# Performance work log

Hardware: AMD Instinct MI355X
Metric: run time of the kernel (lower is better)

## Reference

```python
import jax, jax.numpy as jnp
import numpy as np

B, N, D, H = 8, 512, 1024, 16
HD = D // H
NI = 4          # num_instances == num_instances_per_batch
MAXI = 16       # max_instances
SCALE = HD ** -0.5


def _rms(t, w, eps=1e-6):
    return t * jax.lax.rsqrt(jnp.mean(t * t, axis=-1, keepdims=True) + eps) * w


def _lin(t, W, b):
    return t @ W + b


def _heads(t):
    b, n = t.shape[0], t.shape[1]
    return t.reshape(b, n, H, HD).transpose(0, 2, 1, 3)  # [b, H, n, hd]


def setup_inputs() -> dict:
    key = jax.random.key(0)
    ks = iter(jax.random.split(key, 16))

    def w(shape):
        return jax.random.normal(next(ks), shape, dtype=jnp.float32) * 0.02

    return {
        "x": jax.random.normal(next(ks), (B, N, D), dtype=jnp.float32),
        "instance_mask": jax.random.uniform(next(ks), (B, N, NI), dtype=jnp.float32),
        "Wq": w((D, D)), "bq": jnp.zeros((D,), jnp.float32),
        "Wk": w((D, D)), "bk": jnp.zeros((D,), jnp.float32),
        "Wv": w((D, D)), "bv": jnp.zeros((D,), jnp.float32),
        "Wo": w((D, D)), "bo": jnp.zeros((D,), jnp.float32),
        "Wiq": w((D, D)), "biq": jnp.zeros((D,), jnp.float32),
        "Wik": w((D, D)), "bik": jnp.zeros((D,), jnp.float32),
        "instance_embed": w((1, MAXI, D)),
        "qnorm_w": jnp.ones((HD,), jnp.float32),
        "knorm_w": jnp.ones((HD,), jnp.float32),
        "num_instances": NI,
        "num_instances_per_batch": NI,
    }


def reference(x, instance_mask, Wq, bq, Wk, bk, Wv, bv, Wo, bo,
              Wiq, biq, Wik, bik, instance_embed, qnorm_w, knorm_w,
              num_instances, num_instances_per_batch):
    # QKV projections + per-head QK-RMSNorm
    q = _rms(_heads(_lin(x, Wq, bq)), qnorm_w)   # [B,H,N,hd]
    k = _rms(_heads(_lin(x, Wk, bk)), knorm_w)
    v = _heads(_lin(x, Wv, bv))
    ni = num_instances                           # == num_instances_per_batch here,
    G = B // num_instances_per_batch             # so no leftover self-attn sub-branch;
    # (the module's initial global attention output is overwritten by this branch)
    qg = q.reshape(G, ni, H, N, HD)
    kg = k.reshape(G, ni, H, N, HD).transpose(0, 2, 1, 3, 4).reshape(G, H, ni * N, HD)
    vg = v.reshape(G, ni, H, N, HD).transpose(0, 2, 1, 3, 4).reshape(G, H, ni * N, HD)
    scores = jnp.einsum('gihnd,ghmd->gihnm', qg, kg) * SCALE  # [G,ni,H,N,ni*N]
    p = jax.nn.softmax(scores, axis=-1)
    og = jnp.einsum('gihnm,ghmd->gihnd', p, vg)
    out = og.reshape(B, H, N, HD).transpose(0, 2, 1, 3).reshape(B, N, D)
    # instance-embedding gate
    inst_feat = jnp.einsum('bnk,kd->bnd', instance_mask, instance_embed[0, :ni])
    iq = _heads(_lin(out, Wiq, biq))
    ik = _heads(_lin(inst_feat, Wik, bik))
    # mean over heads folded into the einsum (same math as mean of per-head scores)
    inst_attn = jax.nn.sigmoid(jnp.einsum('bhnd,bhmd->bnm', iq, ik) * (SCALE / H))
    gate = 1.0 + jnp.mean(inst_attn, axis=-1, keepdims=True)  # [B,N,1]
    return _lin(out * gate, Wo, bo)
```

## Files before the change

kernel.cpp:

```cpp
#include <hip/hip_runtime.h>
#include <cmath>

#define B_   8
#define N_   512
#define D_   1024
#define H_   16
#define HD_  64
#define NI_  4
#define BN_  (B_*N_)
#define KVLEN (NI_*N_)

typedef __attribute__((ext_vector_type(8)))  short  bf16x8;
typedef __attribute__((ext_vector_type(8)))  __bf16 bf16x8_t;
typedef __attribute__((ext_vector_type(16))) float  f32x16;
typedef __attribute__((ext_vector_type(4)))  short  s16x4;
typedef __attribute__((ext_vector_type(2)))  unsigned u32x2;

__device__ __forceinline__ short bf16_rn(float x) {
  unsigned u = __float_as_uint(x);
  unsigned r = (u + 0x7FFFu + ((u >> 16) & 1u)) >> 16;
  return (short)r;
}

__device__ __forceinline__ void split2(float x, short& hi, short& lo) {
  hi = bf16_rn(x);
  float h = __uint_as_float(((unsigned)(unsigned short)hi) << 16);
  float r = x - h;
  lo = bf16_rn(r);
}

__device__ __forceinline__ f32x16 mfma_bf16(bf16x8 a, bf16x8 b, f32x16 c) {
  return __builtin_amdgcn_mfma_f32_32x32x16_bf16(
      __builtin_bit_cast(bf16x8_t, a), __builtin_bit_cast(bf16x8_t, b), c, 0, 0, 0);
}

#define GLOAD16(gp, lp) __builtin_amdgcn_global_load_lds( \
  (const __attribute__((address_space(1))) unsigned*)(gp), \
  (__attribute__((address_space(3))) unsigned*)(lp), 16, 0, 0)

__device__ __forceinline__ long tiled_off(int row, int k) {
  return ((((long)(row >> 7) * 128 + (k >> 3)) * 128 + (row & 127)) * 8 + (k & 7));
}

__device__ __forceinline__ void xcd_swizzle(int& bx, int& by, int& bz) {
  const int gx = gridDim.x, gy = gridDim.y;
  const int nwg = gx * gy * gridDim.z;
  const int lin = blockIdx.x + gx * (blockIdx.y + gy * blockIdx.z);
  const int swz = (lin & 7) * (nwg >> 3) + (lin >> 3);
  bx = swz % gx;
  const int rest = swz / gx;
  by = rest % gy;
  bz = rest / gy;
}

__global__ __launch_bounds__(256) void wsplitAll(
    const float* __restrict__ Wq, const float* __restrict__ Wk,
    const float* __restrict__ Wv, const float* __restrict__ Wiq,
    const float* __restrict__ Wik, const float* __restrict__ Wo,
    short* __restrict__ QKVh, short* __restrict__ Gateh)
{
  __shared__ float tile[64][65];
  const int z = blockIdx.z;
  const float* W = (z == 0) ? Wq : (z == 1) ? Wk : (z == 2) ? Wv
                 : (z == 3) ? Wiq : (z == 4) ? Wik : Wo;
  const int t  = threadIdx.x;
  const int kb = blockIdx.y * 64;
  const int cb = blockIdx.x * 64;
  const int r0 = t >> 4;
  const int c4 = t & 15;
  #pragma unroll
  for (int i = 0; i < 4; i++) {
    const int r = r0 + i * 16;
    *(float4*)&tile[r][c4 * 4] = *(const float4*)&W[(long)(kb + r) * D_ + cb + c4 * 4];
  }
  __syncthreads();
  #pragma unroll
  for (int i = 0; i < 4; i++) {
    const int c = r0 + i * 16;
    short hi[4];
    #pragma unroll
    for (int e = 0; e < 4; e++)
      hi[e] = bf16_rn(tile[c4 * 4 + e][c]);
    if (z < 3) {
      *(s16x4*)&QKVh[tiled_off(z * D_ + cb + c, kb + c4 * 4)] = *(s16x4*)hi;
    } else {
      *(s16x4*)&Gateh[(long)(z - 3) * D_ * D_ + tiled_off(cb + c, kb + c4 * 4)] = *(s16x4*)hi;
    }
  }
}

__global__ __launch_bounds__(256) void asplit(const float* __restrict__ in,
                                              short* __restrict__ hi)
{
  const long i4 = ((long)blockIdx.x * 256 + threadIdx.x) * 4;
  const int row = (int)(i4 >> 10);
  const int kk  = (int)(i4 & 1023);
  float4 v = *(const float4*)&in[i4];
  short h[4];
  h[0] = bf16_rn(v.x);
  h[1] = bf16_rn(v.y);
  h[2] = bf16_rn(v.z);
  h[3] = bf16_rn(v.w);
  *(s16x4*)&hi[tiled_off(row, kk)] = *(s16x4*)h;
}

template<int MODE, int SPLIT>
__global__ __launch_bounds__(256) void mfgemm2(
    const short* __restrict__ Ahi, const short* __restrict__ Alo,
    const short* __restrict__ Bhi, const short* __restrict__ Blo,
    const float* __restrict__ b0, const float* __restrict__ b1,
    const float* __restrict__ b2,
    float* __restrict__ C, short* __restrict__ Chi, short* __restrict__ Clo,
    int aBlk, int bBlk, long sC,
    const float* __restrict__ gate_in)
{
  constexpr int NOPS = (SPLIT == 2) ? 3 : 2;
  __shared__ short lds[2][NOPS][4096];
  const int t = threadIdx.x, w = t >> 6, lane = t & 63;
  int bx, by, bz;
  xcd_swizzle(bx, by, bz);
  const int rowBase = by * 128;
  const int colBase = bx * 128;
  const int batch = (MODE == 5) ? (bz >> 1) : bz;
  const long kOff = (MODE == 5) ? (long)(bz & 1) * 65536 : 0;
  const long aoff = (long)(batch * aBlk + by) * 131072 + kOff;
  const long boff = (long)(batch * bBlk + bx) * 131072 + kOff;

  const short* Abase = (MODE == 4 && bz) ? Alo : Ahi;
  const short* Bbase = (MODE == 4 && bz) ? Blo : Bhi;

  const short* mySrc;
  int op, half;
  if (SPLIT == 2) {
    op = (w < 3) ? w : 0; half = 0;
    mySrc = (w == 0) ? Ahi + aoff : (w == 1) ? Alo + aoff : Bhi + boff;
  } else {
    op = w >> 1; half = w & 1;
    mySrc = op ? Bbase + boff : Abase + aoff;
  }

  auto stage = [&](int buf, int tt) {
    if (SPLIT == 2) {
      if (w == 3) return;
      const short* g = mySrc + ((long)tt * 512 + lane) * 8;
      #pragma unroll
      for (int i = 0; i < 8; i++)
        GLOAD16(g + i * 512, &lds[buf][op][i * 512]);
    } else {
      const short* g = mySrc + ((long)tt * 512 + half * 256 + lane) * 8;
      #pragma unroll
      for (int i = 0; i < 4; i++)
        GLOAD16(g + i * 512, &lds[buf][op][(half * 256 + i * 64) * 8]);
    }
  };

  const int wr = w >> 1, wc = w & 1;
  const int lrow = lane & 31, lk = lane >> 5;

  f32x16 acc[2][2] = {};

  auto compute = [&](int buf) {
    #pragma unroll
    for (int kh = 0; kh < 2; kh++) {
      const int kq = 2 * kh + lk;
      bf16x8 ah[2], bh[2];
      #pragma unroll
      for (int m = 0; m < 2; m++)
        ah[m] = *(const bf16x8*)&lds[buf][0][(kq * 128 + wr * 64 + m * 32 + lrow) * 8];
      #pragma unroll
      for (int n = 0; n < 2; n++)
        bh[n] = *(const bf16x8*)&lds[buf][(SPLIT == 2) ? 2 : 1][(kq * 128 + wc * 64 + n * 32 + lrow) * 8];
      if (SPLIT == 2) {
        bf16x8 al[2];
        #pragma unroll
        for (int m = 0; m < 2; m++)
          al[m] = *(const bf16x8*)&lds[buf][1][(kq * 128 + wr * 64 + m * 32 + lrow) * 8];
        #pragma unroll
        for (int m = 0; m < 2; m++)
          #pragma unroll
          for (int n = 0; n < 2; n++) {
            acc[m][n] = mfma_bf16(al[m], bh[n], acc[m][n]);
            acc[m][n] = mfma_bf16(ah[m], bh[n], acc[m][n]);
          }
      } else {
        #pragma unroll
        for (int m = 0; m < 2; m++)
          #pragma unroll
          for (int n = 0; n < 2; n++)
            acc[m][n] = mfma_bf16(ah[m], bh[n], acc[m][n]);
      }
    }
  };

  const int NT = (MODE == 5) ? 16 : 32;
  stage(0, 0);
  for (int tt = 0; tt < NT - 1; ++tt) {
    stage((tt + 1) & 1, tt + 1);
    if (SPLIT == 2) asm volatile("s_waitcnt vmcnt(8)" ::: "memory");
    else            asm volatile("s_waitcnt vmcnt(4)" ::: "memory");
    __builtin_amdgcn_s_barrier();
    __builtin_amdgcn_sched_barrier(0);
    compute(tt & 1);
    __builtin_amdgcn_s_barrier();
  }
  asm volatile("s_waitcnt vmcnt(0)" ::: "memory");
  __builtin_amdgcn_s_barrier();
  __builtin_amdgcn_sched_barrier(0);
  compute((NT - 1) & 1);

  if (MODE == 5) {
    float* Cz = C + (long)(bz & 1) * (8L * 512 * 512) + (long)batch * (512L * 512);
    #pragma unroll
    for (int m = 0; m < 2; m++)
      #pragma unroll
      for (int r = 0; r < 16; r++) {
        const int row = rowBase + wr * 64 + m * 32 + (r & 3) + 8 * (r >> 2) + 4 * lk;
        #pragma unroll
        for (int n = 0; n < 2; n++)
          Cz[(long)row * 512 + colBase + wc * 64 + n * 32 + lrow] = acc[m][n][r];
      }
    return;
  }

  const float* bias = (bz == 1) ? b1 : (bz == 2) ? b2 : b0;
  float bcol[2];
  #pragma unroll
  for (int n = 0; n < 2; n++)
    bcol[n] = bias[colBase + wc * 64 + n * 32 + lrow];

  float* Cb = C + (long)bz * sC;
  short* Cdst = (MODE == 4 && bz) ? Clo : Chi;

  #pragma unroll
  for (int m = 0; m < 2; m++) {
    #pragma unroll
    for (int r = 0; r < 16; r++) {
      const int row = rowBase + wr * 64 + m * 32 + (r & 3) + 8 * (r >> 2) + 4 * lk;
      float g = 1.f;
      if (MODE == 2) g = gate_in[row];
      #pragma unroll
      for (int n = 0; n < 2; n++) {
        const int col = colBase + wc * 64 + n * 32 + lrow;
        const float val = acc[m][n][r] * g + bcol[n];
        if (MODE == 4) {
          Cdst[tiled_off(row, col)] = bf16_rn(val);
        } else {
          Cb[(long)row * D_ + col] = val;
        }
      }
    }
  }
}

__global__ __launch_bounds__(256) void gate_finish(
    const float* __restrict__ zp, float* __restrict__ gate)
{
  const int t = threadIdx.x, w = t >> 6, lane = t & 63;
  const int row = blockIdx.x * 4 + w;
  const float* z0 = zp + (long)row * 512;
  const float* z1 = zp + 8L * 512 * 512 + (long)row * 512;
  const float sc = 0.125f / 16.f;
  float4 a0 = *(const float4*)&z0[lane * 8];
  float4 a1 = *(const float4*)&z0[lane * 8 + 4];
  float4 b0 = *(const float4*)&z1[lane * 8];
  float4 b1 = *(const float4*)&z1[lane * 8 + 4];
  float s = 1.f / (1.f + __expf(-(a0.x + b0.x) * sc))
          + 1.f / (1.f + __expf(-(a0.y + b0.y) * sc))
          + 1.f / (1.f + __expf(-(a0.z + b0.z) * sc))
          + 1.f / (1.f + __expf(-(a0.w + b0.w) * sc))
          + 1.f / (1.f + __expf(-(a1.x + b1.x) * sc))
          + 1.f / (1.f + __expf(-(a1.y + b1.y) * sc))
          + 1.f / (1.f + __expf(-(a1.z + b1.z) * sc))
          + 1.f / (1.f + __expf(-(a1.w + b1.w) * sc));
  #pragma unroll
  for (int m = 1; m < 64; m <<= 1) s += __shfl_xor(s, m);
  if (lane == 0) gate[row] = 1.f + s * (1.f / 512.f);
}

__global__ __launch_bounds__(256) void kvprep(
    const float* __restrict__ kf, const float* __restrict__ vf,
    const float* __restrict__ knw, short* __restrict__ Knb,
    short* __restrict__ Vtb)
{
  const int tile = blockIdx.x, h = blockIdx.y, g = blockIdx.z;
  const int t = threadIdx.x;
  const int skv = t >> 3, sg = t & 7;
  const int m  = tile * 32 + skv;
  const int bb = g * NI_ + (m >> 9), nn = m & (N_ - 1);
  const float* kp = kf + ((long)(bb * N_ + nn)) * D_ + h * HD_ + sg * 8;
  float k8[8];
  *(float4*)&k8[0] = *(const float4*)&kp[0];
  *(float4*)&k8[4] = *(const float4*)&kp[4];
  float ks2 = 0.f;
  #pragma unroll
  for (int j = 0; j < 8; j++) ks2 += k8[j] * k8[j];
  ks2 += __shfl_xor(ks2, 1);
  ks2 += __shfl_xor(ks2, 2);
  ks2 += __shfl_xor(ks2, 4);
  const float kr = rsqrtf(ks2 * (1.f / 64.f) + 1e-6f);
  bf16x8 kb;
  #pragma unroll
  for (int j = 0; j < 8; j++) kb[j] = bf16_rn(k8[j] * kr * knw[sg * 8 + j]);
  *(bf16x8*)&Knb[((long)(g * H_ + h) * KVLEN + m) * 64 + ((sg ^ (m & 7)) * 8)] = kb;
  const int vkv = t & 31, vg = t >> 5;
  const int m2  = tile * 32 + vkv;
  const int bb2 = g * NI_ + (m2 >> 9), nn2 = m2 & (N_ - 1);
  const float* vp = vf + ((long)(bb2 * N_ + nn2)) * D_ + h * HD_ + vg * 8;
  float v8[8];
  *(float4*)&v8[0] = *(const float4*)&vp[0];
  *(float4*)&v8[4] = *(const float4*)&vp[4];
  const long vbase = ((long)(g * H_ + h) * 64 + tile) * 2048;
  #pragma unroll
  for (int e = 0; e < 8; e++) {
    const int d = vg * 8 + e;
    Vtb[vbase + d * 32 + (((vkv >> 3) ^ ((d >> 1) & 3)) * 8) + (vkv & 7)] = bf16_rn(v8[e]);
  }
}

__global__ __launch_bounds__(256) void attn3(
    const float* __restrict__ q, const short* __restrict__ Knb,
    const short* __restrict__ Vtb, const float* __restrict__ qnw,
    float* __restrict__ opart, float* __restrict__ lpart)
{
  int qb, h, bz;
  xcd_swizzle(qb, h, bz);
  const int b  = bz >> 1, s = bz & 1;
  const int g  = b >> 2;
  const int t  = threadIdx.x;
  const int w  = t >> 6;
  const int lane = t & 63;
  const int l31 = lane & 31, hi = lane >> 5;

  __shared__ short Kt[2][2048];
  __shared__ short Vt[2][2048];

  const int qrow = qb * 128 + w * 32 + l31;
  const float* qp = q + ((long)b * N_ + qrow) * D_ + h * HD_ + hi * 8;
  float qv[4][8];
  float ss = 0.f;
  #pragma unroll
  for (int c = 0; c < 4; c++) {
    *(float4*)&qv[c][0] = *(const float4*)&qp[c * 16];
    *(float4*)&qv[c][4] = *(const float4*)&qp[c * 16 + 4];
    #pragma unroll
    for (int j = 0; j < 8; j++) ss += qv[c][j] * qv[c][j];
  }
  ss += __shfl_xor(ss, 32);
  const float qr = rsqrtf(ss * (1.f / 64.f) + 1e-6f);
  bf16x8 qf[4];
  #pragma unroll
  for (int c = 0; c < 4; c++)
    #pragma unroll
    for (int j = 0; j < 8; j++)
      qf[c][j] = bf16_rn(qv[c][j] * qr * qnw[c * 16 + hi * 8 + j]);

  const short* Kg = Knb + (long)(g * H_ + h) * KVLEN * 64 + (long)s * 32 * 2048;
  const short* Vg = Vtb + (long)(g * H_ + h) * 64 * 2048 + (long)s * 32 * 2048;

  auto stage = [&](int buf, int i) {
    GLOAD16(Kg + (long)i * 2048 + t * 8, &Kt[buf][w * 512]);
    GLOAD16(Vg + (long)i * 2048 + t * 8, &Vt[buf][w * 512]);
  };

  f32x16 oacc[2] = {};
  float l = 0.f;

  stage(0, 0);
  for (int i = 0; i < 32; ++i) {
    const int buf = i & 1;
    if (i + 1 < 32) {
      stage(buf ^ 1, i + 1);
      asm volatile("s_waitcnt vmcnt(2)" ::: "memory");
    } else {
      asm volatile("s_waitcnt vmcnt(0)" ::: "memory");
    }
    __builtin_amdgcn_s_barrier();
    __builtin_amdgcn_sched_barrier(0);

    f32x16 sc = {};
    #pragma unroll
    for (int c = 0; c < 4; c++) {
      bf16x8 kfr = *(const bf16x8*)&Kt[buf][l31 * 64 + (((2 * c + hi) * 8) ^ ((l31 & 7) << 3))];
      sc = mfma_bf16(kfr, qf[c], sc);
    }
    float p[16];
    #pragma unroll
    for (int r = 0; r < 16; r++) {
      p[r] = exp2f(fmaf(sc[r], 0.1803368801111244f, -11.541560327111961f));
      l += p[r];
    }
    unsigned wd[8];
    #pragma unroll
    for (int i2 = 0; i2 < 8; i2++)
      asm("v_cvt_pk_bf16_f32 %0, %1, %2" : "=v"(wd[i2]) : "v"(p[2 * i2]), "v"(p[2 * i2 + 1]));
    u32x2 r0 = __builtin_amdgcn_permlane32_swap(wd[0], wd[2], false, false);
    u32x2 r1 = __builtin_amdgcn_permlane32_swap(wd[1], wd[3], false, false);
    u32x2 r2 = __builtin_amdgcn_permlane32_swap(wd[4], wd[6], false, false);
    u32x2 r3 = __builtin_amdgcn_permlane32_swap(wd[5], wd[7], false, false);
    int4 f0 = { (int)r0.x, (int)r1.x, (int)r0.y, (int)r1.y };
    int4 f1 = { (int)r2.x, (int)r3.x, (int)r2.y, (int)r3.y };
    #pragma unroll
    for (int n = 0; n < 2; n++) {
      const int d = n * 32 + l31;
      const int fd = (d >> 1) & 3;
      bf16x8 v0 = *(const bf16x8*)&Vt[buf][d * 32 + ((hi ^ fd) * 8)];
      bf16x8 v1 = *(const bf16x8*)&Vt[buf][d * 32 + (((2 | hi) ^ fd) * 8)];
      oacc[n] = mfma_bf16(__builtin_bit_cast(bf16x8, f0), v0, oacc[n]);
      oacc[n] = mfma_bf16(__builtin_bit_cast(bf16x8, f1), v1, oacc[n]);
    }
    __builtin_amdgcn_s_barrier();
  }

  l += __shfl_xor(l, 32);
  #pragma unroll
  for (int r = 0; r < 16; r++) {
    const int qg = qb * 128 + w * 32 + (r & 3) + 8 * (r >> 2) + 4 * hi;
    float* op = opart + ((long)s * BN_ + b * N_ + qg) * D_ + h * HD_ + l31;
    op[0]  = oacc[0][r];
    op[32] = oacc[1][r];
  }
  if (hi == 0)
    lpart[((long)s * BN_ + b * N_ + qb * 128 + w * 32 + l31) * H_ + h] = l;
}

__global__ __launch_bounds__(256) void reduce_if(
    const float* __restrict__ opart, const float* __restrict__ lpart,
    const float* __restrict__ mask, const float* __restrict__ emb,
    short* __restrict__ ohi, short* __restrict__ olo,
    short* __restrict__ ofh)
{
  const int row = blockIdx.x;
  const int col = threadIdx.x * 4;
  const int h   = col >> 6;
  const float l = lpart[(long)row * H_ + h] + lpart[((long)BN_ + row) * H_ + h];
  const float inv = 1.f / l;
  float4 a = *(const float4*)&opart[(long)row * D_ + col];
  float4 b = *(const float4*)&opart[((long)BN_ + row) * D_ + col];
  short hh[4], ll[4];
  split2((a.x + b.x) * inv, hh[0], ll[0]);
  split2((a.y + b.y) * inv, hh[1], ll[1]);
  split2((a.z + b.z) * inv, hh[2], ll[2]);
  split2((a.w + b.w) * inv, hh[3], ll[3]);
  const long o = tiled_off(row, col);
  *(s16x4*)&ohi[o] = *(s16x4*)hh;
  *(s16x4*)&olo[o] = *(s16x4*)ll;
  const float* mk = mask + (long)row * NI_;
  float4 acc = {0.f, 0.f, 0.f, 0.f};
  #pragma unroll
  for (int i = 0; i < NI_; i++) {
    const float mm = mk[i];
    const float4 e = *(const float4*)&emb[(long)i * D_ + col];
    acc.x = fmaf(mm, e.x, acc.x);
    acc.y = fmaf(mm, e.y, acc.y);
    acc.z = fmaf(mm, e.z, acc.z);
    acc.w = fmaf(mm, e.w, acc.w);
  }
  short fh[4];
  fh[0] = bf16_rn(acc.x);  fh[1] = bf16_rn(acc.y);
  fh[2] = bf16_rn(acc.z);  fh[3] = bf16_rn(acc.w);
  *(s16x4*)&ofh[o] = *(s16x4*)fh;
}

extern "C" void kernel_launch(void* const* d_in, const int* in_sizes, int n_in,
                              void* d_out, int out_size, void* d_ws, size_t ws_size,
                              hipStream_t stream)
{
  const float* x    = (const float*)d_in[0];
  const float* mask = (const float*)d_in[1];
  const float* Wq   = (const float*)d_in[2];
  const float* bq   = (const float*)d_in[3];
  const float* Wk   = (const float*)d_in[4];
  const float* bk   = (const float*)d_in[5];
  const float* Wv   = (const float*)d_in[6];
  const float* bv   = (const float*)d_in[7];
  const float* Wo   = (const float*)d_in[8];
  const float* bo   = (const float*)d_in[9];
  const float* Wiq  = (const float*)d_in[10];
  const float* biq  = (const float*)d_in[11];
  const float* Wik  = (const float*)d_in[12];
  const float* bik  = (const float*)d_in[13];
  const float* emb  = (const float*)d_in[14];
  const float* qnw  = (const float*)d_in[15];
  const float* knw  = (const float*)d_in[16];
  float* out = (float*)d_out;

  float* ws = (float*)d_ws;
  const size_t SZ = (size_t)BN_ * D_;
  float* qbuf = ws;
  float* kbuf = qbuf + SZ;
  float* vbuf = kbuf + SZ;
  float* opart = kbuf;
  short* ohi  = (short*)(vbuf + SZ);
  short* olo  = ohi + SZ;
  short* xhi  = (short*)(ws + 4 * SZ);
  short* xlo  = xhi + SZ;
  short* Knb  = xhi;
  short* Vtb  = xlo;
  float* zpart = (float*)xhi;
  short* Wbig_hi = (short*)(ws + 5 * SZ);
  short* Wbig_lo = Wbig_hi + (size_t)3 * D_ * D_;
  float* gate  = (float*)Wbig_hi;
  float* lpart = gate + BN_;
  short* iqh = (short*)qbuf;
  short* ifh = (short*)qbuf + SZ;
  short* ikh = (short*)vbuf;
  short* WiqH = Wbig_lo;
  short* WikH = Wbig_lo + (size_t)D_ * D_;
  short* WoH  = Wbig_lo + (size_t)2 * D_ * D_;

  const dim3 blk(256);

  wsplitAll<<<dim3(16, 16, 6), blk, 0, stream>>>(
      Wq, Wk, Wv, Wiq, Wik, Wo, Wbig_hi, Wbig_lo);
  asplit<<<(BN_ * D_ / 4) / 256, blk, 0, stream>>>(x, xhi);

  mfgemm2<0, 0><<<dim3(8, 32, 3), blk, 0, stream>>>(
      xhi, nullptr, Wbig_hi, nullptr, bq, bk, bv,
      qbuf, nullptr, nullptr, 0, 8, (long)SZ, nullptr);

  kvprep<<<dim3(KVLEN / 32, H_, 2), blk, 0, stream>>>(kbuf, vbuf, knw, Knb, Vtb);

  attn3<<<dim3(N_ / 128, H_, B_ * 2), blk, 0, stream>>>(
      qbuf, Knb, Vtb, qnw, opart, lpart);

  reduce_if<<<BN_, blk, 0, stream>>>(opart, lpart, mask, emb, ohi, olo, ifh);

  mfgemm2<4, 0><<<dim3(8, 32, 2), blk, 0, stream>>>(
      ohi, ifh, WiqH, WikH, biq, bik, nullptr,
      nullptr, iqh, ikh, 0, 0, 0, nullptr);

  mfgemm2<5, 0><<<dim3(4, 4, 16), blk, 0, stream>>>(
      iqh, nullptr, ikh, nullptr, nullptr, nullptr, nullptr,
      zpart, nullptr, nullptr, 4, 4, 0, nullptr);

  gate_finish<<<BN_ / 4, blk, 0, stream>>>(zpart, gate);

  mfgemm2<2, 2><<<dim3(8, 32, 1), blk, 0, stream>>>(
      ohi, olo, WoH, nullptr, bo, nullptr, nullptr,
      out, nullptr, nullptr, 0, 0, 0, gate);
}
```

Before: 216.7 us.

## Fold instance gate into low-rank projection through Wiq and Wik

Because inst_feat has rank 4 (mask times four embeddings), the gate scores reduce to out·Wiq·(Wik^T·emb^T) plus bias terms. The change precomputes a 1024x5 matrix H5 from the weights in small fp32 kernels, projects the attention output onto it with one GEMV-like pass, then evaluates the sigmoid gate per row against the mask. This removes two large bf16 GEMMs, the batched score GEMM and the weight conversions for Wiq and Wik. In exchange it adds serial, low-parallelism prep kernels (4 and 5 blocks looping over 1024 rows) and changes the rounding path.

```diff
diff --git a/kernel.cpp b/kernel.cpp
--- a/kernel.cpp
+++ b/kernel.cpp
@@ -55,14 +55,12 @@
 
 __global__ __launch_bounds__(256) void wsplitAll(
     const float* __restrict__ Wq, const float* __restrict__ Wk,
-    const float* __restrict__ Wv, const float* __restrict__ Wiq,
-    const float* __restrict__ Wik, const float* __restrict__ Wo,
-    short* __restrict__ QKVh, short* __restrict__ Gateh)
+    const float* __restrict__ Wv, const float* __restrict__ Wo,
+    short* __restrict__ QKVh, short* __restrict__ WoH)
 {
   __shared__ float tile[64][65];
   const int z = blockIdx.z;
-  const float* W = (z == 0) ? Wq : (z == 1) ? Wk : (z == 2) ? Wv
-                 : (z == 3) ? Wiq : (z == 4) ? Wik : Wo;
+  const float* W = (z == 0) ? Wq : (z == 1) ? Wk : (z == 2) ? Wv : Wo;
   const int t  = threadIdx.x;
   const int kb = blockIdx.y * 64;
   const int cb = blockIdx.x * 64;
@@ -81,11 +79,69 @@
     #pragma unroll
     for (int e = 0; e < 4; e++)
       hi[e] = bf16_rn(tile[c4 * 4 + e][c]);
-    if (z < 3) {
+    if (z < 3)
       *(s16x4*)&QKVh[tiled_off(z * D_ + cb + c, kb + c4 * 4)] = *(s16x4*)hi;
-    } else {
-      *(s16x4*)&Gateh[(long)(z - 3) * D_ * D_ + tiled_off(cb + c, kb + c4 * 4)] = *(s16x4*)hi;
-    }
+    else
+      *(s16x4*)&WoH[tiled_off(cb + c, kb + c4 * 4)] = *(s16x4*)hi;
+  }
+}
+
+__global__ __launch_bounds__(256) void fprep(
+    const float* __restrict__ Wik, const float* __restrict__ emb,
+    float* __restrict__ F4)
+{
+  const int d = blockIdx.x * 256 + threadIdx.x;
+  float s0 = 0, s1 = 0, s2 = 0, s3 = 0;
+  for (int e = 0; e < D_; e++) {
+    const float w = Wik[(long)e * D_ + d];
+    s0 = fmaf(emb[e], w, s0);
+    s1 = fmaf(emb[D_ + e], w, s1);
+    s2 = fmaf(emb[2 * D_ + e], w, s2);
+    s3 = fmaf(emb[3 * D_ + e], w, s3);
+  }
+  F4[d] = s0;  F4[D_ + d] = s1;  F4[2 * D_ + d] = s2;  F4[3 * D_ + d] = s3;
+}
+
+__global__ __launch_bounds__(256) void hprep(
+    const float* __restrict__ Wiq, const float* __restrict__ F4,
+    const float* __restrict__ bik, const float* __restrict__ biq,
+    float* __restrict__ H5)
+{
+  const int t = threadIdx.x;
+  if (blockIdx.x < 4) {
+    const int d = blockIdx.x * 256 + t;
+    float s0 = 0, s1 = 0, s2 = 0, s3 = 0, s4 = 0;
+    const float* wr = Wiq + (long)d * D_;
+    for (int e = 0; e < D_; e++) {
+      const float w = wr[e];
+      s0 = fmaf(w, F4[e], s0);
+      s1 = fmaf(w, F4[D_ + e], s1);
+      s2 = fmaf(w, F4[2 * D_ + e], s2);
+      s3 = fmaf(w, F4[3 * D_ + e], s3);
+      s4 = fmaf(w, bik[e], s4);
+    }
+    float* h = &H5[(long)d * 5];
+    h[0] = s0; h[1] = s1; h[2] = s2; h[3] = s3; h[4] = s4;
+  } else {
+    __shared__ float red[256][5];
+    float s0 = 0, s1 = 0, s2 = 0, s3 = 0, s4 = 0;
+    for (int e = t; e < D_; e += 256) {
+      const float b = biq[e];
+      s0 = fmaf(b, F4[e], s0);
+      s1 = fmaf(b, F4[D_ + e], s1);
+      s2 = fmaf(b, F4[2 * D_ + e], s2);
+      s3 = fmaf(b, F4[3 * D_ + e], s3);
+      s4 = fmaf(b, bik[e], s4);
+    }
+    red[t][0] = s0; red[t][1] = s1; red[t][2] = s2; red[t][3] = s3; red[t][4] = s4;
+    __syncthreads();
+    for (int stride = 128; stride > 0; stride >>= 1) {
+      if (t < stride)
+        #pragma unroll
+        for (int j = 0; j < 5; j++) red[t][j] += red[t + stride][j];
+      __syncthreads();
+    }
+    if (t < 5) H5[5120 + t] = red[0][t];
   }
 }
 
@@ -107,11 +163,10 @@
 template<int MODE, int SPLIT>
 __global__ __launch_bounds__(256) void mfgemm2(
     const short* __restrict__ Ahi, const short* __restrict__ Alo,
-    const short* __restrict__ Bhi, const short* __restrict__ Blo,
+    const short* __restrict__ Bhi,
     const float* __restrict__ b0, const float* __restrict__ b1,
     const float* __restrict__ b2,
-    float* __restrict__ C, short* __restrict__ Chi, short* __restrict__ Clo,
-    int aBlk, int bBlk, long sC,
+    float* __restrict__ C, int bBlk, long sC,
     const float* __restrict__ gate_in)
 {
   constexpr int NOPS = (SPLIT == 2) ? 3 : 2;
@@ -121,13 +176,8 @@
   xcd_swizzle(bx, by, bz);
   const int rowBase = by * 128;
   const int colBase = bx * 128;
-  const int batch = (MODE == 5) ? (bz >> 1) : bz;
-  const long kOff = (MODE == 5) ? (long)(bz & 1) * 65536 : 0;
-  const long aoff = (long)(batch * aBlk + by) * 131072 + kOff;
-  const long boff = (long)(batch * bBlk + bx) * 131072 + kOff;
-
-  const short* Abase = (MODE == 4 && bz) ? Alo : Ahi;
-  const short* Bbase = (MODE == 4 && bz) ? Blo : Bhi;
+  const long aoff = (long)by * 131072;
+  const long boff = (long)(bz * bBlk + bx) * 131072;
 
   const short* mySrc;
   int op, half;
@@ -136,7 +186,7 @@
     mySrc = (w == 0) ? Ahi + aoff : (w == 1) ? Alo + aoff : Bhi + boff;
   } else {
     op = w >> 1; half = w & 1;
-    mySrc = op ? Bbase + boff : Abase + aoff;
+    mySrc = op ? Bhi + boff : Ahi + aoff;
   }
 
   auto stage = [&](int buf, int tt) {
@@ -192,7 +242,7 @@
     }
   };
 
-  const int NT = (MODE == 5) ? 16 : 32;
+  const int NT = 32;
   stage(0, 0);
   for (int tt = 0; tt < NT - 1; ++tt) {
     stage((tt + 1) & 1, tt + 1);
@@ -208,20 +258,6 @@
   __builtin_amdgcn_sched_barrier(0);
   compute((NT - 1) & 1);
 
-  if (MODE == 5) {
-    float* Cz = C + (long)(bz & 1) * (8L * 512 * 512) + (long)batch * (512L * 512);
-    #pragma unroll
-    for (int m = 0; m < 2; m++)
-      #pragma unroll
-      for (int r = 0; r < 16; r++) {
-        const int row = rowBase + wr * 64 + m * 32 + (r & 3) + 8 * (r >> 2) + 4 * lk;
-        #pragma unroll
-        for (int n = 0; n < 2; n++)
-          Cz[(long)row * 512 + colBase + wc * 64 + n * 32 + lrow] = acc[m][n][r];
-      }
-    return;
-  }
-
   const float* bias = (bz == 1) ? b1 : (bz == 2) ? b2 : b0;
   float bcol[2];
   #pragma unroll
@@ -229,7 +265,6 @@
     bcol[n] = bias[colBase + wc * 64 + n * 32 + lrow];
 
   float* Cb = C + (long)bz * sC;
-  short* Cdst = (MODE == 4 && bz) ? Clo : Chi;
 
   #pragma unroll
   for (int m = 0; m < 2; m++) {
@@ -241,40 +276,10 @@
       #pragma unroll
       for (int n = 0; n < 2; n++) {
         const int col = colBase + wc * 64 + n * 32 + lrow;
-        const float val = acc[m][n][r] * g + bcol[n];
-        if (MODE == 4) {
-          Cdst[tiled_off(row, col)] = bf16_rn(val);
-        } else {
-          Cb[(long)row * D_ + col] = val;
-        }
+        Cb[(long)row * D_ + col] = acc[m][n][r] * g + bcol[n];
       }
     }
   }
-}
-
-__global__ __launch_bounds__(256) void gate_finish(
-    const float* __restrict__ zp, float* __restrict__ gate)
-{
-  const int t = threadIdx.x, w = t >> 6, lane = t & 63;
-  const int row = blockIdx.x * 4 + w;
-  const float* z0 = zp + (long)row * 512;
-  const float* z1 = zp + 8L * 512 * 512 + (long)row * 512;
-  const float sc = 0.125f / 16.f;
-  float4 a0 = *(const float4*)&z0[lane * 8];
-  float4 a1 = *(const float4*)&z0[lane * 8 + 4];
-  float4 b0 = *(const float4*)&z1[lane * 8];
-  float4 b1 = *(const float4*)&z1[lane * 8 + 4];
-  float s = 1.f / (1.f + __expf(-(a0.x + b0.x) * sc))
-          + 1.f / (1.f + __expf(-(a0.y + b0.y) * sc))
-          + 1.f / (1.f + __expf(-(a0.z + b0.z) * sc))
-          + 1.f / (1.f + __expf(-(a0.w + b0.w) * sc))
-          + 1.f / (1.f + __expf(-(a1.x + b1.x) * sc))
-          + 1.f / (1.f + __expf(-(a1.y + b1.y) * sc))
-          + 1.f / (1.f + __expf(-(a1.z + b1.z) * sc))
-          + 1.f / (1.f + __expf(-(a1.w + b1.w) * sc));
-  #pragma unroll
-  for (int m = 1; m < 64; m <<= 1) s += __shfl_xor(s, m);
-  if (lane == 0) gate[row] = 1.f + s * (1.f / 512.f);
 }
 
 __global__ __launch_bounds__(256) void kvprep(
@@ -423,11 +428,9 @@
     lpart[((long)s * BN_ + b * N_ + qb * 128 + w * 32 + l31) * H_ + h] = l;
 }
 
-__global__ __launch_bounds__(256) void reduce_if(
+__global__ __launch_bounds__(256) void attn_reduce(
     const float* __restrict__ opart, const float* __restrict__ lpart,
-    const float* __restrict__ mask, const float* __restrict__ emb,
-    short* __restrict__ ohi, short* __restrict__ olo,
-    short* __restrict__ ofh)
+    short* __restrict__ ohi, short* __restrict__ olo)
 {
   const int row = blockIdx.x;
   const int col = threadIdx.x * 4;
@@ -444,21 +447,75 @@
   const long o = tiled_off(row, col);
   *(s16x4*)&ohi[o] = *(s16x4*)hh;
   *(s16x4*)&olo[o] = *(s16x4*)ll;
-  const float* mk = mask + (long)row * NI_;
-  float4 acc = {0.f, 0.f, 0.f, 0.f};
-  #pragma unroll
-  for (int i = 0; i < NI_; i++) {
-    const float mm = mk[i];
-    const float4 e = *(const float4*)&emb[(long)i * D_ + col];
-    acc.x = fmaf(mm, e.x, acc.x);
-    acc.y = fmaf(mm, e.y, acc.y);
-    acc.z = fmaf(mm, e.z, acc.z);
-    acc.w = fmaf(mm, e.w, acc.w);
-  }
-  short fh[4];
-  fh[0] = bf16_rn(acc.x);  fh[1] = bf16_rn(acc.y);
-  fh[2] = bf16_rn(acc.z);  fh[3] = bf16_rn(acc.w);
-  *(s16x4*)&ofh[o] = *(s16x4*)fh;
+}
+
+__global__ __launch_bounds__(256) void gproj(
+    const short* __restrict__ ohi, const float* __restrict__ H5,
+    float* __restrict__ G)
+{
+  __shared__ float Hl[5125];
+  __shared__ float gpart[128][5];
+  const int t = threadIdx.x;
+  for (int i = t; i < 5125; i += 256) Hl[i] = H5[i];
+  __syncthreads();
+  const int rb = blockIdx.x;
+  const int row = t & 127, half = t >> 7;
+  float s0 = 0, s1 = 0, s2 = 0, s3 = 0, s4 = 0;
+  const short* base = ohi + (long)rb * 131072 + row * 8;
+  for (int qo = half * 64; qo < half * 64 + 64; qo++) {
+    bf16x8 ov = *(const bf16x8*)&base[qo * 1024];
+    #pragma unroll
+    for (int e = 0; e < 8; e++) {
+      const float of = __uint_as_float(((unsigned)(unsigned short)ov[e]) << 16);
+      const float* hp = &Hl[(qo * 8 + e) * 5];
+      s0 = fmaf(of, hp[0], s0);
+      s1 = fmaf(of, hp[1], s1);
+      s2 = fmaf(of, hp[2], s2);
+      s3 = fmaf(of, hp[3], s3);
+      s4 = fmaf(of, hp[4], s4);
+    }
+  }
+  if (half == 0) {
+    gpart[row][0] = s0; gpart[row][1] = s1; gpart[row][2] = s2;
+    gpart[row][3] = s3; gpart[row][4] = s4;
+  }
+  __syncthreads();
+  if (half == 1) {
+    float* g = &G[(long)(rb * 128 + row) * 5];
+    g[0] = gpart[row][0] + s0 + Hl[5120];
+    g[1] = gpart[row][1] + s1 + Hl[5121];
+    g[2] = gpart[row][2] + s2 + Hl[5122];
+    g[3] = gpart[row][3] + s3 + Hl[5123];
+    g[4] = gpart[row][4] + s4 + Hl[5124];
+  }
+}
+
+__global__ __launch_bounds__(256) void gate_finish2(
+    const float* __restrict__ G, const float* __restrict__ mask,
+    float* __restrict__ gate)
+{
+  __shared__ float mk[512][4];
+  __shared__ float spart[128];
+  const int t = threadIdx.x;
+  const int rb = blockIdx.x;
+  const int batch = rb >> 2;
+  const float* msrc = mask + (long)batch * N_ * NI_;
+  for (int i = t; i < 2048; i += 256) ((float*)mk)[i] = msrc[i];
+  __syncthreads();
+  const int row = t & 127, half = t >> 7;
+  const float* g = &G[(long)(rb * 128 + row) * 5];
+  const float g0 = g[0], g1 = g[1], g2 = g[2], g3 = g[3], g4 = g[4];
+  const float sc = 0.125f / 16.f;
+  float s = 0.f;
+  for (int m = half * 256; m < half * 256 + 256; m++) {
+    const float z = fmaf(g0, mk[m][0], fmaf(g1, mk[m][1],
+                    fmaf(g2, mk[m][2], fmaf(g3, mk[m][3], g4))));
+    s += 1.f / (1.f + __expf(-z * sc));
+  }
+  if (half == 0) spart[row] = s;
+  __syncthreads();
+  if (half == 1)
+    gate[rb * 128 + row] = 1.f + (spart[row] + s) * (1.f / 512.f);
 }
 
 extern "C" void kernel_launch(void* const* d_in, const int* in_sizes, int n_in,
@@ -496,46 +553,39 @@
   short* xlo  = xhi + SZ;
   short* Knb  = xhi;
   short* Vtb  = xlo;
-  float* zpart = (float*)xhi;
   short* Wbig_hi = (short*)(ws + 5 * SZ);
   short* Wbig_lo = Wbig_hi + (size_t)3 * D_ * D_;
   float* gate  = (float*)Wbig_hi;
   float* lpart = gate + BN_;
-  short* iqh = (short*)qbuf;
-  short* ifh = (short*)qbuf + SZ;
-  short* ikh = (short*)vbuf;
-  short* WiqH = Wbig_lo;
-  short* WikH = Wbig_lo + (size_t)D_ * D_;
-  short* WoH  = Wbig_lo + (size_t)2 * D_ * D_;
+  short* WoH = Wbig_lo;
+  float* F4  = (float*)(Wbig_lo + (size_t)D_ * D_);
+  float* H5  = F4 + 4 * D_;
+  float* G   = H5 + 1025 * 5;
 
   const dim3 blk(256);
 
-  wsplitAll<<<dim3(16, 16, 6), blk, 0, stream>>>(
-      Wq, Wk, Wv, Wiq, Wik, Wo, Wbig_hi, Wbig_lo);
+  fprep<<<dim3(4), blk, 0, stream>>>(Wik, emb, F4);
+  hprep<<<dim3(5), blk, 0, stream>>>(Wiq, F4, bik, biq, H5);
+
+  wsplitAll<<<dim3(16, 16, 4), blk, 0, stream>>>(Wq, Wk, Wv, Wo, Wbig_hi, WoH);
   asplit<<<(BN_ * D_ / 4) / 256, blk, 0, stream>>>(x, xhi);
 
   mfgemm2<0, 0><<<dim3(8, 32, 3), blk, 0, stream>>>(
-      xhi, nullptr, Wbig_hi, nullptr, bq, bk, bv,
-      qbuf, nullptr, nullptr, 0, 8, (long)SZ, nullptr);
+      xhi, nullptr, Wbig_hi, bq, bk, bv,
+      qbuf, 8, (long)SZ, nullptr);
 
   kvprep<<<dim3(KVLEN / 32, H_, 2), blk, 0, stream>>>(kbuf, vbuf, knw, Knb, Vtb);
 
   attn3<<<dim3(N_ / 128, H_, B_ * 2), blk, 0, stream>>>(
       qbuf, Knb, Vtb, qnw, opart, lpart);
 
-  reduce_if<<<BN_, blk, 0, stream>>>(opart, lpart, mask, emb, ohi, olo, ifh);
-
-  mfgemm2<4, 0><<<dim3(8, 32, 2), blk, 0, stream>>>(
-      ohi, ifh, WiqH, WikH, biq, bik, nullptr,
-      nullptr, iqh, ikh, 0, 0, 0, nullptr);
-
-  mfgemm2<5, 0><<<dim3(4, 4, 16), blk, 0, stream>>>(
-      iqh, nullptr, ikh, nullptr, nullptr, nullptr, nullptr,
-      zpart, nullptr, nullptr, 4, 4, 0, nullptr);
-
-  gate_finish<<<BN_ / 4, blk, 0, stream>>>(zpart, gate);
+  attn_reduce<<<BN_, blk, 0, stream>>>(opart, lpart, ohi, olo);
+
+  gproj<<<dim3(32), blk, 0, stream>>>(ohi, H5, G);
+
+  gate_finish2<<<dim3(32), blk, 0, stream>>>(G, mask, gate);
 
   mfgemm2<2, 2><<<dim3(8, 32, 1), blk, 0, stream>>>(
-      ohi, olo, WoH, nullptr, bo, nullptr, nullptr,
-      out, nullptr, nullptr, 0, 0, 0, gate);
-}
+      ohi, olo, WoH, bo, nullptr, nullptr,
+      out, 0, 0, gate);
+}
```

Result: slower. 304.2 us (+40.3%).
